# Optimization experiments

Hardware: AMD Instinct MI355X
Metric: run time of the kernel (lower is better)

## Reference

```python
import jax, jax.numpy as jnp
import numpy as np

N_NODES = 50000
N_EDGES = 1600000
D = 64
F = 8
K = 16384


def setup_inputs() -> dict:
    key = jax.random.key(0)
    k1, k2, k3, k4, k5 = jax.random.split(key, 5)
    raw_data = jax.random.randint(k1, (N_NODES,), 0, F, dtype=jnp.int64) if jax.config.jax_enable_x64 else jax.random.randint(k1, (N_NODES,), 0, F, dtype=jnp.int32)
    edge_src = jax.random.randint(k2, (N_EDGES,), 0, N_NODES, dtype=jnp.int32)
    edge_dst = jax.random.randint(k3, (N_EDGES,), 0, N_NODES, dtype=jnp.int32)
    edge_vals = jax.random.normal(k4, (N_EDGES, D), dtype=jnp.float32)
    core_idxs = jax.random.randint(k5, (K,), 0, N_NODES, dtype=jnp.int32)
    return {
        "raw_data": raw_data,
        "edge_src": edge_src,
        "edge_dst": edge_dst,
        "edge_vals": edge_vals,
        "core_idxs": core_idxs,
        "feature_type_count": F,
    }


def reference(raw_data, edge_src, edge_dst, edge_vals, core_idxs, feature_type_count):
    # For each feature type f and origin node i:
    #   out[i, f, :] = max over edges (i -> j) of (edge_vals * [raw_data[j] == f])
    # Origins with no edges at all are zero (torch zero-init of max_res).
    n_nodes = raw_data.shape[0]
    dst_type = raw_data[edge_dst]  # [E] feature type of each edge's neighbor
    outs = []
    for f in range(feature_type_count):  # small fixed loop over feature types
        mask = (dst_type == f).astype(edge_vals.dtype)          # [E]
        masked = edge_vals * mask[:, None]                       # [E, D]
        seg = jax.ops.segment_max(masked, edge_src, num_segments=n_nodes)  # [N, D]
        seg = jnp.where(jnp.isneginf(seg), jnp.zeros((), seg.dtype), seg)  # empty origins -> 0
        outs.append(seg[core_idxs])                              # [K, D]
    return jnp.stack(outs, axis=1)  # [K, F, D]
```

## Files before the change

kernel.cpp:

```cpp
#include <hip/hip_runtime.h>

#define NNODES 50000
#define FT 8
#define DD 64
#define KK 16384
#define CAP 128
#define OVFCAP 32768


__global__ void init_kernel(int* __restrict__ cnt, int* __restrict__ needed,
                            int* __restrict__ head, int* __restrict__ gtot) {
    int i = blockIdx.x * 256 + threadIdx.x;
    if (i < NNODES) { cnt[i] = 0; needed[i] = 0; head[i] = -1; }
    if (i < 4) gtot[i] = 0;
}

__global__ void mark_kernel(const int* __restrict__ core, int* __restrict__ needed,
                            int* __restrict__ head, int* __restrict__ nxt,
                            int* __restrict__ slot_node, int* __restrict__ gtot) {
    int k = blockIdx.x * 256 + threadIdx.x;
    if (k >= KK) return;
    int node = core[k];
    nxt[k] = atomicExch(&head[node], k);
    int old = atomicExch(&needed[node], 1);
    if (!old) {
        int s = atomicAdd(&gtot[1], 1);
        slot_node[s] = node;
    }
}

__global__ void scatter_kernel(const int4* __restrict__ esrc4, const int4* __restrict__ edst4,
                               const int* __restrict__ rawd, const int* __restrict__ needed,
                               int* __restrict__ cnt, int* __restrict__ sorted,
                               int* __restrict__ gtot, int* __restrict__ ovf_node,
                               int* __restrict__ ovf_pk, int nE) {
    int t = blockIdx.x * 256 + threadIdx.x;
    int e = t * 4;
    if (e >= nE) return;
    if (e + 3 < nE) {
        int4 s = esrc4[t];
        int4 d = edst4[t];
        int sv[4] = {s.x, s.y, s.z, s.w};
        int dv[4] = {d.x, d.y, d.z, d.w};
#pragma unroll
        for (int j = 0; j < 4; ++j) {
            int sn = sv[j];
            if (!needed[sn]) continue;
            int pk = ((e + j) << 3) | rawd[dv[j]];
            int p = atomicAdd(&cnt[sn], 1);
            if (p < CAP) {
                sorted[sn * CAP + p] = pk;
            } else {
                int q = atomicAdd(&gtot[0], 1);
                if (q < OVFCAP) { ovf_node[q] = sn; ovf_pk[q] = pk; }
            }
        }
    } else {
        const int* esrc = (const int*)esrc4;
        const int* edst = (const int*)edst4;
        for (; e < nE; ++e) {
            int sn = esrc[e];
            if (!needed[sn]) continue;
            int pk = (e << 3) | rawd[edst[e]];
            int p = atomicAdd(&cnt[sn], 1);
            if (p < CAP) {
                sorted[sn * CAP + p] = pk;
            } else {
                int q = atomicAdd(&gtot[0], 1);
                if (q < OVFCAP) { ovf_node[q] = sn; ovf_pk[q] = pk; }
            }
        }
    }
}

__global__ void compute_kernel(const int* __restrict__ slot_node, const int* __restrict__ cnt,
                               const int* __restrict__ sorted, const int* __restrict__ head,
                               const int* __restrict__ nxt, const float* __restrict__ evals,
                               const int* __restrict__ gtot, const int* __restrict__ ovf_node,
                               const int* __restrict__ ovf_pk, float* __restrict__ out) {
    int wave = (blockIdx.x * blockDim.x + threadIdx.x) >> 6;
    int lane = threadIdx.x & 63;
    if (wave >= gtot[1]) return;
    int node  = __builtin_amdgcn_readfirstlane(slot_node[wave]);
    int deg   = __builtin_amdgcn_readfirstlane(cnt[node]);
    int stored = deg < CAP ? deg : CAP;
    const int4* bkt4 = (const int4*)(sorted + node * CAP);

    float r[FT];
    int   c[FT];
#pragma unroll
    for (int t = 0; t < FT; ++t) { r[t] = -INFINITY; c[t] = 0; }

    int i = 0;
    for (; i + 3 < stored; i += 4) {
        int4 pk4 = bkt4[i >> 2];
        float v0 = evals[(size_t)(pk4.x >> 3) * DD + lane];
        float v1 = evals[(size_t)(pk4.y >> 3) * DD + lane];
        float v2 = evals[(size_t)(pk4.z >> 3) * DD + lane];
        float v3 = evals[(size_t)(pk4.w >> 3) * DD + lane];
        int t0 = pk4.x & 7, t1 = pk4.y & 7, t2 = pk4.z & 7, t3 = pk4.w & 7;
#pragma unroll
        for (int t = 0; t < FT; ++t) {
            bool m0 = (t0 == t); r[t] = m0 ? fmaxf(r[t], v0) : r[t]; c[t] += m0;
            bool m1 = (t1 == t); r[t] = m1 ? fmaxf(r[t], v1) : r[t]; c[t] += m1;
            bool m2 = (t2 == t); r[t] = m2 ? fmaxf(r[t], v2) : r[t]; c[t] += m2;
            bool m3 = (t3 == t); r[t] = m3 ? fmaxf(r[t], v3) : r[t]; c[t] += m3;
        }
    }
    const int* bkt = sorted + node * CAP;
    for (; i < stored; ++i) {
        int pk = bkt[i];
        int tt = pk & 7;
        float v = evals[(size_t)(pk >> 3) * DD + lane];
#pragma unroll
        for (int t = 0; t < FT; ++t) {
            bool m = (tt == t); r[t] = m ? fmaxf(r[t], v) : r[t]; c[t] += m;
        }
    }
    if (deg > CAP) {
        int ovfn = gtot[0]; if (ovfn > OVFCAP) ovfn = OVFCAP;
        for (int j = 0; j < ovfn; ++j) {
            if (ovf_node[j] != node) continue;
            int pk = ovf_pk[j];
            int tt = pk & 7;
            float v = evals[(size_t)(pk >> 3) * DD + lane];
#pragma unroll
            for (int t = 0; t < FT; ++t) {
                bool m = (tt == t); r[t] = m ? fmaxf(r[t], v) : r[t]; c[t] += m;
            }
        }
    }

    float res[FT];
#pragma unroll
    for (int f = 0; f < FT; ++f) {
        int matched = c[f];
        float val;
        if (matched == 0)        val = 0.0f;
        else if (matched < deg)  val = fmaxf(r[f], 0.0f);
        else                     val = r[f];
        res[f] = val;
    }

    for (int k = head[node]; k >= 0; k = nxt[k]) {
        float* op = out + (size_t)k * (FT * DD) + lane;
#pragma unroll
        for (int f = 0; f < FT; ++f) op[f * DD] = res[f];
    }
}

extern "C" void kernel_launch(void* const* d_in, const int* in_sizes, int n_in,
                              void* d_out, int out_size, void* d_ws, size_t ws_size,
                              hipStream_t stream) {
    const int*   rawd  = (const int*)d_in[0];
    const int*   esrc  = (const int*)d_in[1];
    const int*   edst  = (const int*)d_in[2];
    const float* evals = (const float*)d_in[3];
    const int*   core  = (const int*)d_in[4];
    int nE = in_sizes[1];

    int* wsi       = (int*)d_ws;
    int* cnt       = wsi;
    int* needed    = wsi + 50000;
    int* head      = wsi + 100000;
    int* nxt       = wsi + 150000;
    int* slot_node = wsi + 166384;
    int* gtot      = wsi + 182768;
    int* ovf_node  = wsi + 182772;
    int* ovf_pk    = wsi + 215540;
    int* sorted    = wsi + 248320;

    init_kernel<<<(NNODES + 255) / 256, 256, 0, stream>>>(cnt, needed, head, gtot);
    mark_kernel<<<(KK + 255) / 256, 256, 0, stream>>>(core, needed, head, nxt, slot_node, gtot);

    int nE4 = (nE + 3) / 4;
    scatter_kernel<<<(nE4 + 255) / 256, 256, 0, stream>>>(
        (const int4*)esrc, (const int4*)edst, rawd, needed, cnt, sorted,
        gtot, ovf_node, ovf_pk, nE);

    long long cthreads = (long long)KK * 64;
    compute_kernel<<<(int)((cthreads + 255) / 256), 256, 0, stream>>>(
        slot_node, cnt, sorted, head, nxt, evals, gtot, ovf_node, ovf_pk, (float*)d_out);
}
```

Before: 84.61 us.

## Bucket edges per (node, feature type) and pack needed-node flags into a bitset

```diff
diff --git a/kernel.cpp b/kernel.cpp
--- a/kernel.cpp
+++ b/kernel.cpp
@@ -4,36 +4,40 @@
 #define FT 8
 #define DD 64
 #define KK 16384
-#define CAP 128
+#define CAPF 64
 #define OVFCAP 32768
+#define NBW 1568
 
 
-__global__ void init_kernel(int* __restrict__ cnt, int* __restrict__ needed,
+__global__ void init_kernel(int* __restrict__ cnt, int* __restrict__ bits,
                             int* __restrict__ head, int* __restrict__ gtot) {
     int i = blockIdx.x * 256 + threadIdx.x;
-    if (i < NNODES) { cnt[i] = 0; needed[i] = 0; head[i] = -1; }
+    if (i < NNODES * FT) cnt[i] = 0;
+    if (i < NBW) bits[i] = 0;
+    if (i < NNODES) head[i] = -1;
     if (i < 4) gtot[i] = 0;
 }
 
-__global__ void mark_kernel(const int* __restrict__ core, int* __restrict__ needed,
+__global__ void mark_kernel(const int* __restrict__ core, int* __restrict__ bits,
                             int* __restrict__ head, int* __restrict__ nxt,
                             int* __restrict__ slot_node, int* __restrict__ gtot) {
     int k = blockIdx.x * 256 + threadIdx.x;
     if (k >= KK) return;
     int node = core[k];
     nxt[k] = atomicExch(&head[node], k);
-    int old = atomicExch(&needed[node], 1);
-    if (!old) {
+    unsigned bit = 1u << (node & 31);
+    unsigned old = atomicOr((unsigned*)&bits[node >> 5], bit);
+    if (!(old & bit)) {
         int s = atomicAdd(&gtot[1], 1);
         slot_node[s] = node;
     }
 }
 
 __global__ void scatter_kernel(const int4* __restrict__ esrc4, const int4* __restrict__ edst4,
-                               const int* __restrict__ rawd, const int* __restrict__ needed,
+                               const int* __restrict__ rawd, const int* __restrict__ bits,
                                int* __restrict__ cnt, int* __restrict__ sorted,
-                               int* __restrict__ gtot, int* __restrict__ ovf_node,
-                               int* __restrict__ ovf_pk, int nE) {
+                               int* __restrict__ gtot, int* __restrict__ ovf_key,
+                               int* __restrict__ ovf_e, int nE) {
     int t = blockIdx.x * 256 + threadIdx.x;
     int e = t * 4;
     if (e >= nE) return;
@@ -45,14 +49,14 @@
 #pragma unroll
         for (int j = 0; j < 4; ++j) {
             int sn = sv[j];
-            if (!needed[sn]) continue;
-            int pk = ((e + j) << 3) | rawd[dv[j]];
-            int p = atomicAdd(&cnt[sn], 1);
-            if (p < CAP) {
-                sorted[sn * CAP + p] = pk;
+            if (!((((unsigned)bits[sn >> 5]) >> (sn & 31)) & 1u)) continue;
+            int cell = sn * FT + rawd[dv[j]];
+            int p = atomicAdd(&cnt[cell], 1);
+            if (p < CAPF) {
+                sorted[(size_t)cell * CAPF + p] = e + j;
             } else {
                 int q = atomicAdd(&gtot[0], 1);
-                if (q < OVFCAP) { ovf_node[q] = sn; ovf_pk[q] = pk; }
+                if (q < OVFCAP) { ovf_key[q] = cell; ovf_e[q] = e + j; }
             }
         }
     } else {
@@ -60,14 +64,14 @@
         const int* edst = (const int*)edst4;
         for (; e < nE; ++e) {
             int sn = esrc[e];
-            if (!needed[sn]) continue;
-            int pk = (e << 3) | rawd[edst[e]];
-            int p = atomicAdd(&cnt[sn], 1);
-            if (p < CAP) {
-                sorted[sn * CAP + p] = pk;
+            if (!((((unsigned)bits[sn >> 5]) >> (sn & 31)) & 1u)) continue;
+            int cell = sn * FT + rawd[edst[e]];
+            int p = atomicAdd(&cnt[cell], 1);
+            if (p < CAPF) {
+                sorted[(size_t)cell * CAPF + p] = e;
             } else {
                 int q = atomicAdd(&gtot[0], 1);
-                if (q < OVFCAP) { ovf_node[q] = sn; ovf_pk[q] = pk; }
+                if (q < OVFCAP) { ovf_key[q] = cell; ovf_e[q] = e; }
             }
         }
     }
@@ -76,69 +80,69 @@
 __global__ void compute_kernel(const int* __restrict__ slot_node, const int* __restrict__ cnt,
                                const int* __restrict__ sorted, const int* __restrict__ head,
                                const int* __restrict__ nxt, const float* __restrict__ evals,
-                               const int* __restrict__ gtot, const int* __restrict__ ovf_node,
-                               const int* __restrict__ ovf_pk, float* __restrict__ out) {
+                               const int* __restrict__ gtot, const int* __restrict__ ovf_key,
+                               const int* __restrict__ ovf_e, float* __restrict__ out) {
     int wave = (blockIdx.x * blockDim.x + threadIdx.x) >> 6;
     int lane = threadIdx.x & 63;
     if (wave >= gtot[1]) return;
-    int node  = __builtin_amdgcn_readfirstlane(slot_node[wave]);
-    int deg   = __builtin_amdgcn_readfirstlane(cnt[node]);
-    int stored = deg < CAP ? deg : CAP;
-    const int4* bkt4 = (const int4*)(sorted + node * CAP);
+    int node = __builtin_amdgcn_readfirstlane(slot_node[wave]);
 
-    float r[FT];
-    int   c[FT];
+    int cf[FT];
+    int deg = 0;
+    bool anyovf = false;
 #pragma unroll
-    for (int t = 0; t < FT; ++t) { r[t] = -INFINITY; c[t] = 0; }
+    for (int f = 0; f < FT; ++f) {
+        cf[f] = __builtin_amdgcn_readfirstlane(cnt[node * FT + f]);
+        deg += cf[f];
+        anyovf |= (cf[f] > CAPF);
+    }
 
-    int i = 0;
-    for (; i + 3 < stored; i += 4) {
-        int4 pk4 = bkt4[i >> 2];
-        float v0 = evals[(size_t)(pk4.x >> 3) * DD + lane];
-        float v1 = evals[(size_t)(pk4.y >> 3) * DD + lane];
-        float v2 = evals[(size_t)(pk4.z >> 3) * DD + lane];
-        float v3 = evals[(size_t)(pk4.w >> 3) * DD + lane];
-        int t0 = pk4.x & 7, t1 = pk4.y & 7, t2 = pk4.z & 7, t3 = pk4.w & 7;
+    float rmax[FT];
 #pragma unroll
-        for (int t = 0; t < FT; ++t) {
-            bool m0 = (t0 == t); r[t] = m0 ? fmaxf(r[t], v0) : r[t]; c[t] += m0;
-            bool m1 = (t1 == t); r[t] = m1 ? fmaxf(r[t], v1) : r[t]; c[t] += m1;
-            bool m2 = (t2 == t); r[t] = m2 ? fmaxf(r[t], v2) : r[t]; c[t] += m2;
-            bool m3 = (t3 == t); r[t] = m3 ? fmaxf(r[t], v3) : r[t]; c[t] += m3;
+    for (int f = 0; f < FT; ++f) {
+        int n = cf[f] < CAPF ? cf[f] : CAPF;
+        const int* bkt = sorted + ((size_t)node * FT + f) * CAPF;
+        float m0 = -INFINITY, m1 = -INFINITY, m2 = -INFINITY, m3 = -INFINITY;
+        int i = 0;
+        for (; i + 3 < n; i += 4) {
+            int4 q = *(const int4*)(bkt + i);
+            int e0 = __builtin_amdgcn_readfirstlane(q.x);
+            int e1 = __builtin_amdgcn_readfirstlane(q.y);
+            int e2 = __builtin_amdgcn_readfirstlane(q.z);
+            int e3 = __builtin_amdgcn_readfirstlane(q.w);
+            m0 = fmaxf(m0, evals[(size_t)e0 * DD + lane]);
+            m1 = fmaxf(m1, evals[(size_t)e1 * DD + lane]);
+            m2 = fmaxf(m2, evals[(size_t)e2 * DD + lane]);
+            m3 = fmaxf(m3, evals[(size_t)e3 * DD + lane]);
         }
+        for (; i < n; ++i) {
+            int e0 = __builtin_amdgcn_readfirstlane(bkt[i]);
+            m0 = fmaxf(m0, evals[(size_t)e0 * DD + lane]);
+        }
+        rmax[f] = fmaxf(fmaxf(m0, m1), fmaxf(m2, m3));
     }
-    const int* bkt = sorted + node * CAP;
-    for (; i < stored; ++i) {
-        int pk = bkt[i];
-        int tt = pk & 7;
-        float v = evals[(size_t)(pk >> 3) * DD + lane];
+
+    if (anyovf) {
+        int no = gtot[0]; if (no > OVFCAP) no = OVFCAP;
+        for (int q = 0; q < no; ++q) {
+            int key = ovf_key[q];
+            if ((key >> 3) != node) continue;
+            int f = key & 7;
+            float v = evals[(size_t)ovf_e[q] * DD + lane];
 #pragma unroll
-        for (int t = 0; t < FT; ++t) {
-            bool m = (tt == t); r[t] = m ? fmaxf(r[t], v) : r[t]; c[t] += m;
-        }
-    }
-    if (deg > CAP) {
-        int ovfn = gtot[0]; if (ovfn > OVFCAP) ovfn = OVFCAP;
-        for (int j = 0; j < ovfn; ++j) {
-            if (ovf_node[j] != node) continue;
-            int pk = ovf_pk[j];
-            int tt = pk & 7;
-            float v = evals[(size_t)(pk >> 3) * DD + lane];
-#pragma unroll
-            for (int t = 0; t < FT; ++t) {
-                bool m = (tt == t); r[t] = m ? fmaxf(r[t], v) : r[t]; c[t] += m;
-            }
+            for (int t = 0; t < FT; ++t)
+                if (t == f) rmax[t] = fmaxf(rmax[t], v);
         }
     }
 
     float res[FT];
 #pragma unroll
     for (int f = 0; f < FT; ++f) {
-        int matched = c[f];
+        int matched = cf[f];
         float val;
         if (matched == 0)        val = 0.0f;
-        else if (matched < deg)  val = fmaxf(r[f], 0.0f);
-        else                     val = r[f];
+        else if (matched < deg)  val = fmaxf(rmax[f], 0.0f);
+        else                     val = rmax[f];
         res[f] = val;
     }
 
@@ -161,24 +165,24 @@
 
     int* wsi       = (int*)d_ws;
     int* cnt       = wsi;
-    int* needed    = wsi + 50000;
-    int* head      = wsi + 100000;
-    int* nxt       = wsi + 150000;
-    int* slot_node = wsi + 166384;
-    int* gtot      = wsi + 182768;
-    int* ovf_node  = wsi + 182772;
-    int* ovf_pk    = wsi + 215540;
-    int* sorted    = wsi + 248320;
+    int* bits      = wsi + 400000;
+    int* head      = wsi + 401568;
+    int* nxt       = wsi + 451568;
+    int* slot_node = wsi + 467952;
+    int* gtot      = wsi + 484336;
+    int* ovf_key   = wsi + 484340;
+    int* ovf_e     = wsi + 517108;
+    int* sorted    = wsi + 549888;
 
-    init_kernel<<<(NNODES + 255) / 256, 256, 0, stream>>>(cnt, needed, head, gtot);
-    mark_kernel<<<(KK + 255) / 256, 256, 0, stream>>>(core, needed, head, nxt, slot_node, gtot);
+    init_kernel<<<(NNODES * FT + 255) / 256, 256, 0, stream>>>(cnt, bits, head, gtot);
+    mark_kernel<<<(KK + 255) / 256, 256, 0, stream>>>(core, bits, head, nxt, slot_node, gtot);
 
     int nE4 = (nE + 3) / 4;
     scatter_kernel<<<(nE4 + 255) / 256, 256, 0, stream>>>(
-        (const int4*)esrc, (const int4*)edst, rawd, needed, cnt, sorted,
-        gtot, ovf_node, ovf_pk, nE);
+        (const int4*)esrc, (const int4*)edst, rawd, bits, cnt, sorted,
+        gtot, ovf_key, ovf_e, nE);
 
     long long cthreads = (long long)KK * 64;
     compute_kernel<<<(int)((cthreads + 255) / 256), 256, 0, stream>>>(
-        slot_node, cnt, sorted, head, nxt, evals, gtot, ovf_node, ovf_pk, (float*)d_out);
+        slot_node, cnt, sorted, head, nxt, evals, gtot, ovf_key, ovf_e, (float*)d_out);
 }
```

New measurement: 75.88 us. 10.3% less time.
